# Optimization experiments

Measured on AMD Instinct MI355X. Metric: run time of the kernel, lower is better.

## Reference

```python
import jax, jax.numpy as jnp
import numpy as np

RATIO = 5            # neg_sample_ratio -> k
THRESH = 0.1         # hard_neg_threshold
SMOOTH = 0.1         # label_smoothing
FILL = -1.0e9        # masked-fill value for invalid negatives


def _l2norm(x):
    # F.normalize(p=2, dim=-1) with eps=1e-12 clamp on the norm
    n = jnp.linalg.norm(x, axis=-1, keepdims=True)
    return x / jnp.maximum(n, 1e-12)


def setup_inputs() -> dict:
    key = jax.random.key(0)
    k1, k2, k3, k4 = jax.random.split(key, 4)
    N, D, B = 100_000, 256, 4096
    memory = jax.random.normal(k1, (N, D), dtype=jnp.float32)
    src_nodes = jax.random.randint(k2, (B,), 0, N)
    dst_nodes = jax.random.randint(k3, (B,), 0, N)
    labels = jnp.ones((B,), dtype=jnp.float32)          # all positive -> num_pos = B (static)
    timestamps = jax.random.uniform(k4, (B,), dtype=jnp.float32)
    return {"src_nodes": src_nodes, "dst_nodes": dst_nodes, "labels": labels,
            "timestamps": timestamps, "memory": memory}


def reference(src_nodes, dst_nodes, labels, timestamps, memory):
    N = memory.shape[0]
    B = src_nodes.shape[0]
    k = RATIO                                # min(ratio, N-1) with N >> ratio
    M = B * k                                # target_count = num_pos * ratio

    pos_mask = labels == 1.0                 # all True for this setup (static num_pos)

    # normalized cosine-similarity matmul  [B, N]
    mem_n = _l2norm(memory)
    src_n = mem_n[src_nodes]
    sim = src_n @ mem_n.T

    # ground-truth + threshold masking
    cols = jnp.arange(N)[None, :]
    valid = (cols != dst_nodes[:, None]) & (sim > THRESH) & pos_mask[:, None]
    score = jnp.where(valid, sim, FILL) + 1.0    # weights = ones

    # top-k hard-negative mining
    topk_vals, topk_idx = jax.lax.top_k(score, k)    # [B, k]
    is_real = topk_vals > FILL + 1.0

    # flatten row-major (matches repeat_interleave / reshape(-1))
    flat_src = jnp.repeat(src_nodes, k)
    flat_ts = jnp.repeat(timestamps, k)
    flat_dst = topk_idx.reshape(-1)
    flat_real = is_real.reshape(-1)

    # stable sort: real negatives first (== boolean-mask filter order), pads last
    order = jnp.argsort(jnp.logical_not(flat_real), stable=True)
    s_src, s_dst, s_ts = flat_src[order], flat_dst[order], flat_ts[order]

    # random fill for positions beyond current_count (fixed total size M)
    cur = flat_real.sum()
    pos = jnp.arange(M)
    fill_i = jnp.clip(pos - cur, 0, M - 1)
    rand_dst = jax.random.randint(jax.random.key(42), (M,), 0, N)
    r_src = flat_src[fill_i]
    r_ts = flat_ts[fill_i]
    r_dst = rand_dst[fill_i]
    r_dst = jnp.where(r_dst == r_src, (r_dst + 1) % N, r_dst)  # collision fix

    need = pos >= cur
    final_src = jnp.where(need, r_src, s_src)
    final_dst = jnp.where(need, r_dst, s_dst)
    final_ts = jnp.where(need, r_ts, s_ts)

    # assemble augmented batch + label smoothing
    new_src = jnp.concatenate([src_nodes, final_src])
    new_dst = jnp.concatenate([dst_nodes, final_dst])
    new_ts = jnp.concatenate([timestamps, final_ts])
    new_labels = jnp.concatenate([labels, jnp.zeros((M,), jnp.float32)])
    new_labels = new_labels * (1.0 - SMOOTH) + (1.0 - new_labels) * SMOOTH
    return new_src, new_dst, new_labels, new_ts, topk_vals
```

## Files before the change

kernel.cpp:

```cpp
#include <hip/hip_runtime.h>

#define D 256
#define BM 128
#define BN 128
#define BK 64
#define CAP 512
#define KTOP 5
#define T0 0.20f
#define NEGFILL (-1.0e9f)

typedef short bf16x8 __attribute__((ext_vector_type(8)));
typedef float f32x4 __attribute__((ext_vector_type(4)));

#define GLOAD_LDS16(gp, lp)                                                    \
  __builtin_amdgcn_global_load_lds(                                            \
      (const __attribute__((address_space(1))) unsigned int*)(gp),             \
      (__attribute__((address_space(3))) unsigned int*)(lp), 16, 0, 0)

__device__ inline unsigned short f2bf(float x) {
  unsigned u = __builtin_bit_cast(unsigned, x);
  unsigned r = u + 0x7fffu + ((u >> 16) & 1u);
  return (unsigned short)(r >> 16);
}

__global__ __launch_bounds__(256) void kinit(const float* __restrict__ mem,
                                             unsigned short* __restrict__ memn,
                                             float* __restrict__ invn,
                                             const int* __restrict__ srcn,
                                             unsigned short* __restrict__ Apack,
                                             int* __restrict__ cnt,
                                             int N, int B, int NB1) {
  int warp = threadIdx.x >> 6, lane = threadIdx.x & 63;
  if ((int)blockIdx.x < NB1) {
    int row = blockIdx.x * 4 + warp;
    if (row >= N) return;
    float4 v = *(const float4*)(mem + (size_t)row * D + lane * 4);
    float ss = v.x * v.x + v.y * v.y + v.z * v.z + v.w * v.w;
#pragma unroll
    for (int m = 1; m < 64; m <<= 1) ss += __shfl_xor(ss, m);
    float inv = 1.0f / fmaxf(sqrtf(ss), 1e-12f);
    if (lane == 0) invn[row] = inv;
    ushort4 o;
    o.x = f2bf(v.x * inv); o.y = f2bf(v.y * inv);
    o.z = f2bf(v.z * inv); o.w = f2bf(v.w * inv);
    *(ushort4*)(memn + (size_t)row * D + lane * 4) = o;
  } else {
    int row = (blockIdx.x - NB1) * 4 + warp;
    if (row >= B) return;
    int s = srcn[row];
    float4 v = *(const float4*)(mem + (size_t)s * D + lane * 4);
    float ss = v.x * v.x + v.y * v.y + v.z * v.z + v.w * v.w;
#pragma unroll
    for (int m = 1; m < 64; m <<= 1) ss += __shfl_xor(ss, m);
    float inv = 1.0f / fmaxf(sqrtf(ss), 1e-12f);
    ushort4 o;
    o.x = f2bf(v.x * inv); o.y = f2bf(v.y * inv);
    o.z = f2bf(v.z * inv); o.w = f2bf(v.w * inv);
    *(ushort4*)(Apack + (size_t)row * D + lane * 4) = o;
    if (lane == 0) cnt[row] = 0;
  }
}

__global__ __launch_bounds__(256, 4) void kgemm(const unsigned short* __restrict__ Apack,
                                                const unsigned short* __restrict__ memn,
                                                int* __restrict__ cnt,
                                                int* __restrict__ cand,
                                                int B, int N, int MB) {
  __shared__ __align__(16) unsigned short lA[BM * BK];
  __shared__ __align__(16) unsigned short lB[BN * BK];
  int bx = blockIdx.x;
  int nwg = gridDim.x;
  if ((nwg & 7) == 0) {
    bx = (bx & 7) * (nwg >> 3) + (bx >> 3);
  }
  int cb = bx / MB, rb = bx % MB;
  int t = threadIdx.x;
  int w = t >> 6, lane = t & 63;
  int wm = w >> 1, wn = w & 1;
  int lr = lane & 15, lk = lane >> 4;

  int srow = w * 8 + (lane >> 3);
  int q = (lane & 7) ^ (lane >> 3);
  const unsigned short* gA = Apack + (size_t)(rb * BM + srow) * D + q * 8;
  const unsigned short* gB = memn + (size_t)(cb * BN + srow) * D + q * 8;
  unsigned short* lAw = lA + w * 512 + lane * 8;
  unsigned short* lBw = lB + w * 512 + lane * 8;

  f32x4 acc[4][4];
#pragma unroll
  for (int i = 0; i < 4; ++i)
#pragma unroll
    for (int j = 0; j < 4; ++j) acc[i][j] = {0.f, 0.f, 0.f, 0.f};

  for (int kc = 0; kc < 4; ++kc) {
    if (kc) __syncthreads();
#pragma unroll
    for (int i = 0; i < 4; ++i)
      GLOAD_LDS16(gA + (size_t)i * 32 * D + kc * BK, lAw + i * 2048);
#pragma unroll
    for (int i = 0; i < 4; ++i)
      GLOAD_LDS16(gB + (size_t)i * 32 * D + kc * BK, lBw + i * 2048);
    __syncthreads();
#pragma unroll
    for (int kk = 0; kk < 2; ++kk) {
      bf16x8 af[4], bfr[4];
#pragma unroll
      for (int i = 0; i < 4; ++i) {
        int row = wm * 64 + i * 16 + lr;
        int p = (kk * 4 + lk) ^ (row & 7);
        af[i] = *(const bf16x8*)(lA + row * BK + p * 8);
      }
#pragma unroll
      for (int j = 0; j < 4; ++j) {
        int row = wn * 64 + j * 16 + lr;
        int p = (kk * 4 + lk) ^ (row & 7);
        bfr[j] = *(const bf16x8*)(lB + row * BK + p * 8);
      }
#pragma unroll
      for (int i = 0; i < 4; ++i)
#pragma unroll
        for (int j = 0; j < 4; ++j)
          acc[i][j] = __builtin_amdgcn_mfma_f32_16x16x32_bf16(af[i], bfr[j], acc[i][j], 0, 0, 0);
    }
  }

  int rowbase = rb * BM + wm * 64;
  int colbase = cb * BN + wn * 64;
#pragma unroll
  for (int i = 0; i < 4; ++i)
#pragma unroll
    for (int j = 0; j < 4; ++j)
#pragma unroll
      for (int r = 0; r < 4; ++r) {
        float v = acc[i][j][r];
        int grow = rowbase + i * 16 + lk * 4 + r;
        int gcol = colbase + j * 16 + lr;
        if (v > T0 && gcol < N && grow < B) {
          int p = atomicAdd(&cnt[grow], 1);
          if (p < CAP) cand[(size_t)grow * CAP + p] = gcol;
        }
      }
}

__global__ __launch_bounds__(256) void krescore(const float* __restrict__ mem,
                                                const float* __restrict__ invn,
                                                const int* __restrict__ srcn,
                                                const int* __restrict__ dstn,
                                                const float* __restrict__ labels,
                                                const int* __restrict__ cnt,
                                                const int* __restrict__ cand,
                                                float* __restrict__ out_topk,
                                                int* __restrict__ topidx,
                                                int* __restrict__ nreal, int N) {
  __shared__ __align__(16) float srow[D];
  __shared__ float svals[CAP];
  __shared__ int scols[CAP];
  int row = blockIdx.x;
  int t = threadIdx.x, lane = t & 63;
  int g = t >> 4, l16 = t & 15;
  int src = srcn[row], dst = dstn[row];
  bool rowok = (labels[row] == 1.0f);
  float inv_s = invn[src];
  if (t < 64) *(float4*)(srow + t * 4) = *(const float4*)(mem + (size_t)src * D + t * 4);
  int n = cnt[row]; if (n > CAP) n = CAP;
  __syncthreads();
  for (int c = g; c < n; c += 16) {
    int col = cand[(size_t)row * CAP + c];
    const float4* vp = (const float4*)(mem + (size_t)col * D);
    float s = 0.f;
#pragma unroll
    for (int j = 0; j < 4; ++j) {
      float4 v = vp[j * 16 + l16];
      float4 u = *(const float4*)(srow + (j * 16 + l16) * 4);
      s += v.x * u.x + v.y * u.y + v.z * u.z + v.w * u.w;
    }
#pragma unroll
    for (int m = 1; m < 16; m <<= 1) s += __shfl_xor(s, m);
    if (l16 == 0) {
      float sim = s * inv_s * invn[col];
      bool valid = rowok && (col != dst) && (sim > 0.1f);
      svals[c] = valid ? sim : -2.0f;
      scols[c] = col;
    }
  }
  __syncthreads();
  if (t < 64) {
    int reals = 0;
    for (int it = 0; it < KTOP; ++it) {
      float bv = -3.0f; int bc = 0x7fffffff; int bp = -1;
      for (int c = lane; c < n; c += 64) {
        float v = svals[c]; int col = scols[c];
        if (v > bv || (v == bv && col < bc)) { bv = v; bc = col; bp = c; }
      }
#pragma unroll
      for (int m = 1; m < 64; m <<= 1) {
        float ov = __shfl_xor(bv, m); int oc = __shfl_xor(bc, m); int op = __shfl_xor(bp, m);
        if (ov > bv || (ov == bv && oc < bc)) { bv = ov; bc = oc; bp = op; }
      }
      if (lane == 0) {
        if (bv > 0.0f) {
          out_topk[row * KTOP + it] = bv + 1.0f;
          topidx[row * KTOP + it] = bc;
          reals++;
        } else {
          out_topk[row * KTOP + it] = NEGFILL + 1.0f;
          topidx[row * KTOP + it] = 0;
        }
        if (bp >= 0) svals[bp] = -3.0f;
      }
      __asm__ volatile("" ::: "memory");
    }
    if (lane == 0) nreal[row] = reals;
  }
}

__global__ __launch_bounds__(1024) void kfinal(const int* __restrict__ srcn,
                                               const int* __restrict__ dstn,
                                               const float* __restrict__ labels,
                                               const float* __restrict__ ts,
                                               const int* __restrict__ topidx,
                                               const int* __restrict__ nreal,
                                               float* __restrict__ out, int B, int M) {
  __shared__ int lsum[1024];
  __shared__ int rp[4096];
  int t = threadIdx.x;
  int per = (B + 1023) / 1024;
  int base = t * per;
  int c = 0;
  for (int i = 0; i < per; ++i) {
    int f = base + i;
    if (f < B) c += nreal[f];
  }
  lsum[t] = c;
  __syncthreads();
  for (int s = 1; s < 1024; s <<= 1) {
    int add = (t >= s) ? lsum[t - s] : 0;
    __syncthreads();
    lsum[t] += add;
    __syncthreads();
  }
  int run = lsum[t] - c;
  for (int i = 0; i < per; ++i) {
    int f = base + i;
    if (f < B) { rp[f] = run; run += nreal[f]; }
  }
  __syncthreads();
  int cur = lsum[1023];
  int S = B + M;
  for (int x = t; x < B; x += 1024) {
    float lab = labels[x];
    out[x] = (float)srcn[x];
    out[S + x] = (float)dstn[x];
    out[2 * S + x] = lab * 0.9f + (1.0f - lab) * 0.1f;
    out[3 * S + x] = ts[x];
  }
  for (int x = t; x < M; x += 1024) {
    int row = x / KTOP;
    int i = x - row * KTOP;
    int nr = nreal[row], rpr = rp[row];
    bool real = i < nr;
    int p = real ? (rpr + i) : (cur + (row * KTOP - rpr) + (i - nr));
    out[B + p] = (float)srcn[row];
    out[S + B + p] = (float)topidx[x];
    out[2 * S + B + x] = 0.1f;
    out[3 * S + B + p] = ts[row];
  }
}

__global__ __launch_bounds__(1024) void kscan(const int* __restrict__ nreal,
                                              int* __restrict__ rpre, int B) {
  __shared__ int lsum[1024];
  int t = threadIdx.x;
  int per = (B + 1023) / 1024;
  int base = t * per;
  int c = 0;
  for (int i = 0; i < per; ++i) {
    int f = base + i;
    if (f < B) c += nreal[f];
  }
  lsum[t] = c;
  __syncthreads();
  for (int s = 1; s < 1024; s <<= 1) {
    int add = (t >= s) ? lsum[t - s] : 0;
    __syncthreads();
    lsum[t] += add;
    __syncthreads();
  }
  int run = lsum[t] - c;
  for (int i = 0; i < per; ++i) {
    int f = base + i;
    if (f < B) { rpre[f] = run; run += nreal[f]; }
  }
  if (t == 1023) rpre[B] = lsum[1023];
}

__global__ __launch_bounds__(256) void kwrite(const int* __restrict__ srcn,
                                              const int* __restrict__ dstn,
                                              const float* __restrict__ labels,
                                              const float* __restrict__ ts,
                                              const int* __restrict__ topidx,
                                              const int* __restrict__ nreal,
                                              const int* __restrict__ rpre,
                                              float* __restrict__ out, int B, int M) {
  int t = blockIdx.x * 256 + threadIdx.x;
  int S = B + M;
  if (t < B) {
    float lab = labels[t];
    out[t] = (float)srcn[t];
    out[S + t] = (float)dstn[t];
    out[2 * S + t] = lab * 0.9f + (1.0f - lab) * 0.1f;
    out[3 * S + t] = ts[t];
  }
  if (t < M) {
    int row = t / KTOP;
    int i = t - row * KTOP;
    int nr = nreal[row], rp = rpre[row], cur = rpre[B];
    bool real = i < nr;
    int p = real ? (rp + i) : (cur + (row * KTOP - rp) + (i - nr));
    out[B + p] = (float)srcn[row];
    out[S + B + p] = (float)topidx[t];
    out[2 * S + B + t] = 0.1f;
    out[3 * S + B + p] = ts[row];
  }
}

extern "C" void kernel_launch(void* const* d_in, const int* in_sizes, int n_in,
                              void* d_out, int out_size, void* d_ws, size_t ws_size,
                              hipStream_t stream) {
  const int* srcn = (const int*)d_in[0];
  const int* dstn = (const int*)d_in[1];
  const float* labels = (const float*)d_in[2];
  const float* ts = (const float*)d_in[3];
  const float* mem = (const float*)d_in[4];
  int B = in_sizes[0];
  int N = in_sizes[4] / D;
  int M = B * KTOP;
  float* out = (float*)d_out;

  char* w = (char*)d_ws;
  unsigned short* memn = (unsigned short*)w; w += (size_t)N * D * 2;
  float* invn = (float*)w;                   w += (size_t)N * 4;
  unsigned short* Apack = (unsigned short*)w; w += (size_t)B * D * 2;
  int* cnt = (int*)w;                        w += (size_t)B * 4;
  int* cand = (int*)w;                       w += (size_t)B * CAP * 4;
  int* topidx = (int*)w;                     w += (size_t)B * KTOP * 4;
  int* nreal = (int*)w;                      w += (size_t)B * 4;
  int* rpre = (int*)w;                       w += (size_t)(B + 1) * 4;

  int NB1 = (N + 3) / 4;
  kinit<<<NB1 + (B + 3) / 4, 256, 0, stream>>>(mem, memn, invn, srcn, Apack,
                                               cnt, N, B, NB1);
  int MB = (B + BM - 1) / BM;
  int NB = (N + BN - 1) / BN;
  kgemm<<<MB * NB, 256, 0, stream>>>(Apack, memn, cnt, cand, B, N, MB);
  krescore<<<B, 256, 0, stream>>>(mem, invn, srcn, dstn, labels, cnt, cand,
                                  out + 4 * (size_t)(B + M), topidx, nreal, N);
  if (B <= 4096) {
    kfinal<<<1, 1024, 0, stream>>>(srcn, dstn, labels, ts, topidx, nreal,
                                   out, B, M);
  } else {
    kscan<<<1, 1024, 0, stream>>>(nreal, rpre, B);
    kwrite<<<(M + 255) / 256, 256, 0, stream>>>(srcn, dstn, labels, ts, topidx,
                                                nreal, rpre, out, B, M);
  }
}
```

Measured before the change: 447.8 us.

## Fuse final compaction into rescore via last-block tail and move positive-row writes

Removes the separate single-block kfinal launch by having the last krescore block to finish (found with a global atomic counter and threadfences) run the prefix scan and scatter. The positive-row output writes move into kinit's source-row branch. This saves one kernel launch and its gap, but the tail now runs on one 256-thread block instead of 1024 threads. Every krescore block also pays an extra barrier and an atomic, and the 16KB rp shared array raises LDS use per block, which may lower krescore occupancy.

```diff
diff --git a/kernel.cpp b/kernel.cpp
--- a/kernel.cpp
+++ b/kernel.cpp
@@ -27,9 +27,15 @@
                                              unsigned short* __restrict__ memn,
                                              float* __restrict__ invn,
                                              const int* __restrict__ srcn,
+                                             const int* __restrict__ dstn,
+                                             const float* __restrict__ labels,
+                                             const float* __restrict__ ts,
                                              unsigned short* __restrict__ Apack,
                                              int* __restrict__ cnt,
-                                             int N, int B, int NB1) {
+                                             int* __restrict__ done,
+                                             float* __restrict__ out,
+                                             int N, int B, int M, int NB1) {
+  if (blockIdx.x == 0 && threadIdx.x == 0) *done = 0;
   int warp = threadIdx.x >> 6, lane = threadIdx.x & 63;
   if ((int)blockIdx.x < NB1) {
     int row = blockIdx.x * 4 + warp;
@@ -57,7 +63,15 @@
     o.x = f2bf(v.x * inv); o.y = f2bf(v.y * inv);
     o.z = f2bf(v.z * inv); o.w = f2bf(v.w * inv);
     *(ushort4*)(Apack + (size_t)row * D + lane * 4) = o;
-    if (lane == 0) cnt[row] = 0;
+    if (lane == 0) {
+      cnt[row] = 0;
+      int S = B + M;
+      float lab = labels[row];
+      out[row] = (float)s;
+      out[S + row] = (float)dstn[row];
+      out[2 * S + row] = lab * 0.9f + (1.0f - lab) * 0.1f;
+      out[3 * S + row] = ts[row];
+    }
   }
 }
 
@@ -147,14 +161,21 @@
                                                 const int* __restrict__ srcn,
                                                 const int* __restrict__ dstn,
                                                 const float* __restrict__ labels,
+                                                const float* __restrict__ ts,
                                                 const int* __restrict__ cnt,
                                                 const int* __restrict__ cand,
                                                 float* __restrict__ out_topk,
                                                 int* __restrict__ topidx,
-                                                int* __restrict__ nreal, int N) {
+                                                int* __restrict__ nreal,
+                                                int* __restrict__ done,
+                                                float* __restrict__ out,
+                                                int N, int B, int M, int doTail) {
   __shared__ __align__(16) float srow[D];
   __shared__ float svals[CAP];
   __shared__ int scols[CAP];
+  __shared__ int rp[4096];
+  __shared__ int lsum2[256];
+  __shared__ int lastS;
   int row = blockIdx.x;
   int t = threadIdx.x, lane = t & 63;
   int g = t >> 4, l16 = t & 15;
@@ -212,58 +233,49 @@
     }
     if (lane == 0) nreal[row] = reals;
   }
-}
-
-__global__ __launch_bounds__(1024) void kfinal(const int* __restrict__ srcn,
-                                               const int* __restrict__ dstn,
-                                               const float* __restrict__ labels,
-                                               const float* __restrict__ ts,
-                                               const int* __restrict__ topidx,
-                                               const int* __restrict__ nreal,
-                                               float* __restrict__ out, int B, int M) {
-  __shared__ int lsum[1024];
-  __shared__ int rp[4096];
-  int t = threadIdx.x;
-  int per = (B + 1023) / 1024;
+  if (!doTail) return;
+  __syncthreads();
+  if (t == 0) {
+    __threadfence();
+    lastS = (atomicAdd(done, 1) == (int)gridDim.x - 1);
+  }
+  __syncthreads();
+  if (!lastS) return;
+  __threadfence();
+
+  int per = (B + 255) / 256;
   int base = t * per;
-  int c = 0;
+  int c2 = 0;
   for (int i = 0; i < per; ++i) {
     int f = base + i;
-    if (f < B) c += nreal[f];
-  }
-  lsum[t] = c;
-  __syncthreads();
-  for (int s = 1; s < 1024; s <<= 1) {
-    int add = (t >= s) ? lsum[t - s] : 0;
-    __syncthreads();
-    lsum[t] += add;
-    __syncthreads();
-  }
-  int run = lsum[t] - c;
+    if (f < B) c2 += nreal[f];
+  }
+  lsum2[t] = c2;
+  __syncthreads();
+  for (int s = 1; s < 256; s <<= 1) {
+    int add = (t >= s) ? lsum2[t - s] : 0;
+    __syncthreads();
+    lsum2[t] += add;
+    __syncthreads();
+  }
+  int run = lsum2[t] - c2;
   for (int i = 0; i < per; ++i) {
     int f = base + i;
     if (f < B) { rp[f] = run; run += nreal[f]; }
   }
   __syncthreads();
-  int cur = lsum[1023];
+  int cur = lsum2[255];
   int S = B + M;
-  for (int x = t; x < B; x += 1024) {
-    float lab = labels[x];
-    out[x] = (float)srcn[x];
-    out[S + x] = (float)dstn[x];
-    out[2 * S + x] = lab * 0.9f + (1.0f - lab) * 0.1f;
-    out[3 * S + x] = ts[x];
-  }
-  for (int x = t; x < M; x += 1024) {
-    int row = x / KTOP;
-    int i = x - row * KTOP;
-    int nr = nreal[row], rpr = rp[row];
+  for (int x = t; x < M; x += 256) {
+    int r2 = x / KTOP;
+    int i = x - r2 * KTOP;
+    int nr = nreal[r2], rpr = rp[r2];
     bool real = i < nr;
-    int p = real ? (rpr + i) : (cur + (row * KTOP - rpr) + (i - nr));
-    out[B + p] = (float)srcn[row];
+    int p = real ? (rpr + i) : (cur + (r2 * KTOP - rpr) + (i - nr));
+    out[B + p] = (float)srcn[r2];
     out[S + B + p] = (float)topidx[x];
     out[2 * S + B + x] = 0.1f;
-    out[3 * S + B + p] = ts[row];
+    out[3 * S + B + p] = ts[r2];
   }
 }
 
@@ -304,13 +316,6 @@
                                               float* __restrict__ out, int B, int M) {
   int t = blockIdx.x * 256 + threadIdx.x;
   int S = B + M;
-  if (t < B) {
-    float lab = labels[t];
-    out[t] = (float)srcn[t];
-    out[S + t] = (float)dstn[t];
-    out[2 * S + t] = lab * 0.9f + (1.0f - lab) * 0.1f;
-    out[3 * S + t] = ts[t];
-  }
   if (t < M) {
     int row = t / KTOP;
     int i = t - row * KTOP;
@@ -346,19 +351,20 @@
   int* topidx = (int*)w;                     w += (size_t)B * KTOP * 4;
   int* nreal = (int*)w;                      w += (size_t)B * 4;
   int* rpre = (int*)w;                       w += (size_t)(B + 1) * 4;
+  int* done = (int*)w;                       w += 64;
 
   int NB1 = (N + 3) / 4;
-  kinit<<<NB1 + (B + 3) / 4, 256, 0, stream>>>(mem, memn, invn, srcn, Apack,
-                                               cnt, N, B, NB1);
+  kinit<<<NB1 + (B + 3) / 4, 256, 0, stream>>>(mem, memn, invn, srcn, dstn,
+                                               labels, ts, Apack, cnt, done,
+                                               out, N, B, M, NB1);
   int MB = (B + BM - 1) / BM;
   int NB = (N + BN - 1) / BN;
   kgemm<<<MB * NB, 256, 0, stream>>>(Apack, memn, cnt, cand, B, N, MB);
-  krescore<<<B, 256, 0, stream>>>(mem, invn, srcn, dstn, labels, cnt, cand,
-                                  out + 4 * (size_t)(B + M), topidx, nreal, N);
-  if (B <= 4096) {
-    kfinal<<<1, 1024, 0, stream>>>(srcn, dstn, labels, ts, topidx, nreal,
-                                   out, B, M);
-  } else {
+  int doTail = (B <= 4096);
+  krescore<<<B, 256, 0, stream>>>(mem, invn, srcn, dstn, labels, ts, cnt, cand,
+                                  out + 4 * (size_t)(B + M), topidx, nreal,
+                                  done, out, N, B, M, doTail);
+  if (!doTail) {
     kscan<<<1, 1024, 0, stream>>>(nreal, rpre, B);
     kwrite<<<(M + 255) / 256, 256, 0, stream>>>(srcn, dstn, labels, ts, topidx,
                                                 nreal, rpre, out, B, M);
```

Measured after the change: 548.1 us. 22.4% more time.
